# Optimization experiments

Measured on AMD Instinct MI355X. Metric: run time of the kernel, lower is better.

## Reference

```python
import jax, jax.numpy as jnp
import numpy as np

NUM_HEADS = 64
NUM_HEADS_KV = 1
HEAD_SIZE = 64
HIDDEN = NUM_HEADS * HEAD_SIZE  # 4096
SOFTMAX_SCALE = HEAD_SIZE ** -0.5
BATCH = 4
SEQ = 1024
TOTAL = BATCH * SEQ


def setup_inputs() -> dict:
    key = jax.random.key(0)
    k1, k2, k3, k4, k5 = jax.random.split(key, 5)
    hidden_states = jax.random.normal(k1, (TOTAL, HIDDEN), dtype=jnp.float32)
    # rotary cos/sin per token position (head_size/2 features, rotate-half style)
    pos = jnp.tile(jnp.arange(SEQ, dtype=jnp.float32), BATCH)  # [TOTAL]
    inv_freq = 1.0 / (10000.0 ** (jnp.arange(0, HEAD_SIZE, 2, dtype=jnp.float32) / HEAD_SIZE))
    freqs = pos[:, None] * inv_freq[None, :]  # [TOTAL, 32]
    cos = jnp.cos(freqs)
    sin = jnp.sin(freqs)
    w_qkv = jax.random.normal(k2, (HIDDEN, HIDDEN + 2 * NUM_HEADS_KV * HEAD_SIZE), dtype=jnp.float32) * (HIDDEN ** -0.5)
    w_dense = jax.random.normal(k3, (HIDDEN, HIDDEN), dtype=jnp.float32) * (HIDDEN ** -0.5)
    cu_seqlen_prefill = jnp.arange(BATCH + 1, dtype=jnp.int32) * SEQ
    return {
        "hidden_states": hidden_states,
        "cos": cos,
        "sin": sin,
        "w_qkv": w_qkv,
        "w_dense": w_dense,
        "cu_seqlen_prefill": cu_seqlen_prefill,
    }


def _rope(x, cos, sin):
    # x: [T, H, D]; cos/sin: [T, D/2]; rotate-half pairing (x1=first half, x2=second half)
    d2 = x.shape[-1] // 2
    x1, x2 = x[..., :d2], x[..., d2:]
    c = cos[:, None, :]
    s = sin[:, None, :]
    return jnp.concatenate([x1 * c - x2 * s, x2 * c + x1 * s], axis=-1)


def reference(hidden_states, cos, sin, w_qkv, w_dense, cu_seqlen_prefill):
    T = hidden_states.shape[0]
    B = cu_seqlen_prefill.shape[0] - 1
    S = T // B
    qkv = hidden_states @ w_qkv  # [T, H*D + 2*D]
    q = qkv[:, : NUM_HEADS * HEAD_SIZE].reshape(T, NUM_HEADS, HEAD_SIZE)
    kv = qkv[:, NUM_HEADS * HEAD_SIZE:].reshape(T, 2, NUM_HEADS_KV, HEAD_SIZE)
    k = kv[:, 0]  # [T, 1, D]
    v = kv[:, 1]
    q = _rope(q, cos, sin)
    k = _rope(k, cos, sin)
    # ragged sequences of equal length -> batch view (prefill flash-attn path, causal)
    qb = q.reshape(B, S, NUM_HEADS, HEAD_SIZE)
    kb = k.reshape(B, S, NUM_HEADS_KV, HEAD_SIZE)[:, :, 0]  # MQA: single kv head [B,S,D]
    vb = v.reshape(B, S, NUM_HEADS_KV, HEAD_SIZE)[:, :, 0]
    scores = jnp.einsum("bshd,btd->bhst", qb, kb) * SOFTMAX_SCALE  # [B,H,S,S]
    causal = jnp.tril(jnp.ones((S, S), dtype=bool))
    scores = jnp.where(causal[None, None], scores, jnp.finfo(scores.dtype).min)
    p = jax.nn.softmax(scores, axis=-1)
    out = jnp.einsum("bhst,btd->bshd", p, vb)  # [B,S,H,D]
    out = out.reshape(T, NUM_HEADS * HEAD_SIZE)
    return out @ w_dense
```

## Files before the change

kernel.cpp:

```cpp
#include <hip/hip_runtime.h>
#include <hip/hip_bf16.h>
#include <stdint.h>

#define HID   4096
#define NQKV  4224
#define TOT   4096
#define SEQq  1024
#define NH    64
#define HD    64
#define SM_SCALE 0.125f
#define LOG2E 1.44269504088896f

typedef float  f32x4  __attribute__((ext_vector_type(4)));
typedef short  short8 __attribute__((ext_vector_type(8)));
typedef ushort ushort4v __attribute__((ext_vector_type(4)));

static __device__ __forceinline__ ushort f2bf(float f) {
    uint32_t u = __float_as_uint(f);
    u += 0x7FFFu + ((u >> 16) & 1u);
    return (ushort)(u >> 16);
}

static __device__ __forceinline__ void gload_lds16(const void* g, void* l) {
    __builtin_amdgcn_global_load_lds(
        (const __attribute__((address_space(1))) uint32_t*)g,
        (__attribute__((address_space(3))) uint32_t*)l, 16, 0, 0);
}

__global__ __launch_bounds__(256) void cast_bf16_kernel(
    const float* __restrict__ in, ushort* __restrict__ out, int n4)
{
    int i = blockIdx.x * 256 + threadIdx.x;
    if (i < n4) {
        float4 v = ((const float4*)in)[i];
        ushort4v o;
        o.x = f2bf(v.x); o.y = f2bf(v.y); o.z = f2bf(v.z); o.w = f2bf(v.w);
        ((ushort4v*)out)[i] = o;
    }
}

__global__ __launch_bounds__(256) void transpose_cast_kernel(
    const float* __restrict__ in, ushort* __restrict__ out, int R, int C)
{
    __shared__ float tile[32][33];
    int c0 = blockIdx.x * 32, r0 = blockIdx.y * 32;
    int tx = threadIdx.x & 31, ty = threadIdx.x >> 5;
#pragma unroll
    for (int i = 0; i < 4; i++)
        tile[ty + i * 8][tx] = in[(size_t)(r0 + ty + i * 8) * C + c0 + tx];
    __syncthreads();
#pragma unroll
    for (int i = 0; i < 4; i++)
        out[(size_t)(c0 + ty + i * 8) * R + r0 + tx] = f2bf(tile[tx][ty + i * 8]);
}

template<int EPI>
__global__ __launch_bounds__(256) void gemm_kernel(
    const ushort* __restrict__ A, const ushort* __restrict__ B,
    float* __restrict__ Cf, ushort* __restrict__ qkv, ushort* __restrict__ vt,
    const float* __restrict__ cosT, const float* __restrict__ sinT,
    int M, int N, int K)
{
    __shared__ char lds[32768];
    char* ldsA = lds;
    char* ldsB = lds + 16384;
    const int lane = threadIdx.x & 63, wave = threadIdx.x >> 6;
    const int wm = wave >> 1, wn = wave & 1;
    const int m0 = blockIdx.y * 128, n0 = blockIdx.x * 128;

    f32x4 acc[4][4] = {};

    const int srow = lane >> 3;
    const int scol = ((lane & 7) ^ srow) << 3;

    for (int k0 = 0; k0 < K; k0 += 64) {
#pragma unroll
        for (int c = 0; c < 4; c++) {
            int rA = (c * 4 + wave) * 8 + srow;
            gload_lds16(A + (size_t)(m0 + rA) * K + k0 + scol,
                        ldsA + (c * 4 + wave) * 1024);
            gload_lds16(B + (size_t)(n0 + rA) * K + k0 + scol,
                        ldsB + (c * 4 + wave) * 1024);
        }
        __syncthreads();
#pragma unroll
        for (int s = 0; s < 2; s++) {
            const int cb = (s * 64 + ((lane >> 4) << 4)) ^ ((lane & 7) << 4);
            short8 af[4], bfr[4];
#pragma unroll
            for (int m = 0; m < 4; m++)
                af[m] = *(const short8*)(ldsA + (wm * 64 + m * 16 + (lane & 15)) * 128 + cb);
#pragma unroll
            for (int n = 0; n < 4; n++)
                bfr[n] = *(const short8*)(ldsB + (wn * 64 + n * 16 + (lane & 15)) * 128 + cb);
#pragma unroll
            for (int m = 0; m < 4; m++)
#pragma unroll
                for (int n = 0; n < 4; n++)
                    acc[m][n] = __builtin_amdgcn_mfma_f32_16x16x32_bf16(
                        af[m], bfr[n], acc[m][n], 0, 0, 0);
        }
        __syncthreads();
    }

    if (EPI == 0) {
#pragma unroll
        for (int m = 0; m < 4; m++) {
            int row = m0 + wm * 64 + m * 16 + ((lane >> 4) << 2);
#pragma unroll
            for (int n = 0; n < 4; n++) {
                int col = n0 + wn * 64 + n * 16 + (lane & 15);
#pragma unroll
                for (int j = 0; j < 4; j++)
                    Cf[(size_t)(row + j) * N + col] = acc[m][n][j];
            }
        }
    } else {
        const int cn = n0 + wn * 64;
        if (cn < HID + HD) {
#pragma unroll
            for (int m = 0; m < 4; m++)
#pragma unroll
                for (int j = 0; j < 4; j++) {
                    int t = m0 + wm * 64 + m * 16 + ((lane >> 4) << 2) + j;
#pragma unroll
                    for (int n = 0; n < 2; n++) {
                        int d = n * 16 + (lane & 15);
                        float c = cosT[t * 32 + d];
                        float s = sinT[t * 32 + d];
                        float x1 = acc[m][n][j], x2 = acc[m][n + 2][j];
                        qkv[(size_t)t * NQKV + cn + d]      = f2bf(x1 * c - x2 * s);
                        qkv[(size_t)t * NQKV + cn + d + 32] = f2bf(x2 * c + x1 * s);
                    }
                }
        } else {
#pragma unroll
            for (int m = 0; m < 4; m++)
#pragma unroll
                for (int n = 0; n < 4; n++)
#pragma unroll
                    for (int j = 0; j < 4; j++) {
                        int t = m0 + wm * 64 + m * 16 + ((lane >> 4) << 2) + j;
                        int d = n * 16 + (lane & 15);
                        vt[(size_t)((t >> 10) * 64 + d) * SEQq + (t & 1023)] =
                            f2bf(acc[m][n][j]);
                    }
        }
    }
}

__global__ __launch_bounds__(256) void attn_kernel(
    const ushort* __restrict__ qkv, const ushort* __restrict__ vt,
    ushort* __restrict__ aout)
{
    __shared__ char plds[16384];
    const int lane = threadIdx.x & 63, wave = threadIdx.x >> 6;
    const int qb = blockIdx.x, h = blockIdx.y, b = blockIdx.z;
    const int q0 = qb * 128 + wave * 32;
    char* pbase = plds + wave * 4096;

    short8 aq[2][2];
#pragma unroll
    for (int m = 0; m < 2; m++)
#pragma unroll
        for (int ks = 0; ks < 2; ks++)
            aq[m][ks] = *(const short8*)(qkv +
                (size_t)(b * SEQq + q0 + m * 16 + (lane & 15)) * NQKV +
                h * HD + ks * 32 + ((lane >> 4) << 3));

    f32x4 o[2][4] = {};
    float Lp[2][4] = {};
    const float Cs = SM_SCALE * LOG2E;

    const int kvend = q0 + 32;
    for (int kv0 = 0; kv0 < kvend; kv0 += 64) {
        f32x4 sc[2][4] = {};
#pragma unroll
        for (int ks = 0; ks < 2; ks++) {
            short8 bk[4];
#pragma unroll
            for (int n = 0; n < 4; n++)
                bk[n] = *(const short8*)(qkv +
                    (size_t)(b * SEQq + kv0 + n * 16 + (lane & 15)) * NQKV +
                    HID + ks * 32 + ((lane >> 4) << 3));
#pragma unroll
            for (int m = 0; m < 2; m++)
#pragma unroll
                for (int n = 0; n < 4; n++)
                    sc[m][n] = __builtin_amdgcn_mfma_f32_16x16x32_bf16(
                        aq[m][ks], bk[n], sc[m][n], 0, 0, 0);
        }
#pragma unroll
        for (int m = 0; m < 2; m++)
#pragma unroll
            for (int n = 0; n < 4; n++) {
                int kvg = kv0 + n * 16 + (lane & 15);
#pragma unroll
                for (int j = 0; j < 4; j++) {
                    int qg = q0 + m * 16 + ((lane >> 4) << 2) + j;
                    float e = __builtin_amdgcn_exp2f(sc[m][n][j] * Cs);
                    float p = (kvg <= qg) ? e : 0.f;
                    Lp[m][j] += p;
                    int qq = m * 16 + ((lane >> 4) << 2) + j;
                    *(ushort*)(pbase + qq * 128 +
                        (((n * 16 + (lane & 15)) * 2) ^ ((qq & 7) << 4))) = f2bf(p);
                }
            }
#pragma unroll
        for (int ks2 = 0; ks2 < 2; ks2++) {
            short8 pa[2], vb[4];
#pragma unroll
            for (int m = 0; m < 2; m++)
                pa[m] = *(const short8*)(pbase + (m * 16 + (lane & 15)) * 128 +
                    ((ks2 * 64 + ((lane >> 4) << 4)) ^ ((lane & 7) << 4)));
#pragma unroll
            for (int n = 0; n < 4; n++)
                vb[n] = *(const short8*)(vt +
                    (size_t)(b * 64 + n * 16 + (lane & 15)) * SEQq +
                    kv0 + ks2 * 32 + ((lane >> 4) << 3));
#pragma unroll
            for (int m = 0; m < 2; m++)
#pragma unroll
                for (int n = 0; n < 4; n++)
                    o[m][n] = __builtin_amdgcn_mfma_f32_16x16x32_bf16(
                        pa[m], vb[n], o[m][n], 0, 0, 0);
        }
    }

#pragma unroll
    for (int m = 0; m < 2; m++)
#pragma unroll
        for (int j = 0; j < 4; j++) {
            float L = Lp[m][j];
            L += __shfl_xor(L, 1);
            L += __shfl_xor(L, 2);
            L += __shfl_xor(L, 4);
            L += __shfl_xor(L, 8);
            float inv = 1.f / L;
            int t = b * SEQq + q0 + m * 16 + ((lane >> 4) << 2) + j;
#pragma unroll
            for (int n = 0; n < 4; n++)
                aout[(size_t)t * HID + h * HD + n * 16 + (lane & 15)] =
                    f2bf(o[m][n][j] * inv);
        }
}

extern "C" void kernel_launch(void* const* d_in, const int* in_sizes, int n_in,
                              void* d_out, int out_size, void* d_ws, size_t ws_size,
                              hipStream_t stream)
{
    const float* hidden  = (const float*)d_in[0];
    const float* cosT    = (const float*)d_in[1];
    const float* sinT    = (const float*)d_in[2];
    const float* w_qkv   = (const float*)d_in[3];
    const float* w_dense = (const float*)d_in[4];
    float* out = (float*)d_out;

    char* ws = (char*)d_ws;
    ushort* hB   = (ushort*)(ws);
    ushort* wqT  = (ushort*)(ws + 33554432);
    ushort* wdT  = (ushort*)(ws + 68157440);
    ushort* qkvB = (ushort*)(ws + 101711872);
    ushort* vtB  = (ushort*)(ws + 136314880);
    ushort* aoB  = (ushort*)(ws + 136839168);

    cast_bf16_kernel<<<16384, 256, 0, stream>>>(hidden, hB, TOT * HID / 4);
    transpose_cast_kernel<<<dim3(NQKV / 32, HID / 32), 256, 0, stream>>>(
        w_qkv, wqT, HID, NQKV);
    transpose_cast_kernel<<<dim3(HID / 32, HID / 32), 256, 0, stream>>>(
        w_dense, wdT, HID, HID);
    gemm_kernel<1><<<dim3(NQKV / 128, TOT / 128), 256, 0, stream>>>(
        hB, wqT, nullptr, qkvB, vtB, cosT, sinT, TOT, NQKV, HID);
    attn_kernel<<<dim3(8, NH, 4), 256, 0, stream>>>(qkvB, vtB, aoB);
    gemm_kernel<0><<<dim3(HID / 128, TOT / 128), 256, 0, stream>>>(
        aoB, wdT, out, nullptr, nullptr, nullptr, nullptr, TOT, HID, HID);
}
```

Before: 843.7 us.

## Rewrite GEMM with 256x128 tiles, triple-buffered async LDS loads, XCD-aware block remap

Both projection GEMMs now use 512-thread blocks computing 256x128 output tiles. A three-stage LDS ring is filled with direct global-to-LDS loads issued two k-steps ahead and synchronised by vmcnt waits plus one barrier per step, replacing the old single-buffer load/sync/compute loop. The grid is one-dimensional and remapped so consecutive tiles land on the same XCD for L2 reuse, and MFMA sections run at raised wave priority. The larger LDS footprint (144KB) limits occupancy to one block per CU, and the epilogue row mapping must match the new 8-wave layout.

```diff
diff --git a/kernel.cpp b/kernel.cpp
--- a/kernel.cpp
+++ b/kernel.cpp
@@ -54,54 +54,85 @@
         out[(size_t)(c0 + ty + i * 8) * R + r0 + tx] = f2bf(tile[tx][ty + i * 8]);
 }
 
+#define BUFSZ 49152
 template<int EPI>
-__global__ __launch_bounds__(256) void gemm_kernel(
+__global__ __launch_bounds__(512, 1) void gemm2_kernel(
     const ushort* __restrict__ A, const ushort* __restrict__ B,
     float* __restrict__ Cf, ushort* __restrict__ qkv, ushort* __restrict__ vt,
     const float* __restrict__ cosT, const float* __restrict__ sinT,
-    int M, int N, int K)
-{
-    __shared__ char lds[32768];
-    char* ldsA = lds;
-    char* ldsB = lds + 16384;
-    const int lane = threadIdx.x & 63, wave = threadIdx.x >> 6;
+    int M, int N, int K, int MB)
+{
+    extern __shared__ char lds[];
+    const int tid = threadIdx.x;
+    const int lane = tid & 63, wave = tid >> 6;
     const int wm = wave >> 1, wn = wave & 1;
-    const int m0 = blockIdx.y * 128, n0 = blockIdx.x * 128;
+
+    const int nwg = gridDim.x;
+    const int cpx = nwg >> 3;
+    const int id2 = (blockIdx.x & 7) * cpx + (blockIdx.x >> 3);
+    const int by = id2 % MB, bx = id2 / MB;
+    const int m0 = by * 256, n0 = bx * 128;
 
     f32x4 acc[4][4] = {};
 
-    const int srow = lane >> 3;
-    const int scol = ((lane & 7) ^ srow) << 3;
-
-    for (int k0 = 0; k0 < K; k0 += 64) {
-#pragma unroll
-        for (int c = 0; c < 4; c++) {
-            int rA = (c * 4 + wave) * 8 + srow;
-            gload_lds16(A + (size_t)(m0 + rA) * K + k0 + scol,
-                        ldsA + (c * 4 + wave) * 1024);
-            gload_lds16(B + (size_t)(n0 + rA) * K + k0 + scol,
-                        ldsB + (c * 4 + wave) * 1024);
-        }
-        __syncthreads();
-#pragma unroll
-        for (int s = 0; s < 2; s++) {
-            const int cb = (s * 64 + ((lane >> 4) << 4)) ^ ((lane & 7) << 4);
-            short8 af[4], bfr[4];
+    const int srow = tid >> 3;
+    const int scw  = ((tid & 7) ^ (srow & 7)) << 3;
+    const ushort* Abase = A + (size_t)m0 * K;
+    const ushort* Bbase = B + (size_t)n0 * K;
+    const int NT = K >> 6;
+
+#define STAGE(t)  {                                                          \
+        char* buf = lds + ((t) % 3) * BUFSZ;                                 \
+        const int k0 = (t) << 6;                                             \
+        _Pragma("unroll")                                                    \
+        for (int a = 0; a < 4; a++)                                          \
+            gload_lds16(Abase + (size_t)(a * 64 + srow) * K + k0 + scw,      \
+                        buf + a * 8192 + wave * 1024);                       \
+        _Pragma("unroll")                                                    \
+        for (int b2 = 0; b2 < 2; b2++)                                       \
+            gload_lds16(Bbase + (size_t)(b2 * 64 + srow) * K + k0 + scw,     \
+                        buf + 32768 + b2 * 8192 + wave * 1024);              \
+    }
+
+    STAGE(0);
+    STAGE(1);
+
+    for (int t = 0; t < NT; t++) {
+        if (t + 1 < NT)
+            asm volatile("s_waitcnt vmcnt(6)" ::: "memory");
+        else
+            asm volatile("s_waitcnt vmcnt(0)" ::: "memory");
+        __builtin_amdgcn_s_barrier();
+        asm volatile("" ::: "memory");
+        if (t + 2 < NT) STAGE(t + 2);
+
+        const char* bufA = lds + (t % 3) * BUFSZ;
+        const char* bufB = bufA + 32768;
+        short8 af[4][2], bfr[4][2];
+#pragma unroll
+        for (int ks = 0; ks < 2; ks++) {
+            const int cb = (ks * 64 + ((lane >> 4) << 4)) ^ ((lane & 7) << 4);
 #pragma unroll
             for (int m = 0; m < 4; m++)
-                af[m] = *(const short8*)(ldsA + (wm * 64 + m * 16 + (lane & 15)) * 128 + cb);
+                af[m][ks] = *(const short8*)(bufA +
+                    (wm * 64 + m * 16 + (lane & 15)) * 128 + cb);
 #pragma unroll
             for (int n = 0; n < 4; n++)
-                bfr[n] = *(const short8*)(ldsB + (wn * 64 + n * 16 + (lane & 15)) * 128 + cb);
+                bfr[n][ks] = *(const short8*)(bufB +
+                    (wn * 64 + n * 16 + (lane & 15)) * 128 + cb);
+        }
+        __builtin_amdgcn_s_setprio(1);
+#pragma unroll
+        for (int ks = 0; ks < 2; ks++)
 #pragma unroll
             for (int m = 0; m < 4; m++)
 #pragma unroll
                 for (int n = 0; n < 4; n++)
                     acc[m][n] = __builtin_amdgcn_mfma_f32_16x16x32_bf16(
-                        af[m], bfr[n], acc[m][n], 0, 0, 0);
-        }
-        __syncthreads();
-    }
+                        af[m][ks], bfr[n][ks], acc[m][n], 0, 0, 0);
+        __builtin_amdgcn_s_setprio(0);
+    }
+#undef STAGE
 
     if (EPI == 0) {
 #pragma unroll
@@ -264,14 +295,19 @@
     ushort* vtB  = (ushort*)(ws + 136314880);
     ushort* aoB  = (ushort*)(ws + 136839168);
 
+    hipFuncSetAttribute((const void*)gemm2_kernel<1>,
+                        hipFuncAttributeMaxDynamicSharedMemorySize, 3 * BUFSZ);
+    hipFuncSetAttribute((const void*)gemm2_kernel<0>,
+                        hipFuncAttributeMaxDynamicSharedMemorySize, 3 * BUFSZ);
+
     cast_bf16_kernel<<<16384, 256, 0, stream>>>(hidden, hB, TOT * HID / 4);
     transpose_cast_kernel<<<dim3(NQKV / 32, HID / 32), 256, 0, stream>>>(
         w_qkv, wqT, HID, NQKV);
     transpose_cast_kernel<<<dim3(HID / 32, HID / 32), 256, 0, stream>>>(
         w_dense, wdT, HID, HID);
-    gemm_kernel<1><<<dim3(NQKV / 128, TOT / 128), 256, 0, stream>>>(
-        hB, wqT, nullptr, qkvB, vtB, cosT, sinT, TOT, NQKV, HID);
+    gemm2_kernel<1><<<528, 512, 3 * BUFSZ, stream>>>(
+        hB, wqT, nullptr, qkvB, vtB, cosT, sinT, TOT, NQKV, HID, TOT / 256);
     attn_kernel<<<dim3(8, NH, 4), 256, 0, stream>>>(qkvB, vtB, aoB);
-    gemm_kernel<0><<<dim3(HID / 128, TOT / 128), 256, 0, stream>>>(
-        aoB, wdT, out, nullptr, nullptr, nullptr, nullptr, TOT, HID, HID);
-}
+    gemm2_kernel<0><<<512, 512, 3 * BUFSZ, stream>>>(
+        aoB, wdT, out, nullptr, nullptr, nullptr, nullptr, TOT, HID, HID, TOT / 256);
+}
```

Result: faster. 779.8 us (-7.6%).
